# Performance work log

Measured on AMD Instinct MI355X. Metric: run time of the kernel, lower is better.

Reference implementation:

```python
import jax, jax.numpy as jnp
import numpy as np

N_NODES = 100000
N_EDGES = 3200000
F_IN, F_HID, F_OUT = 1433, 8, 7
K = 2  # kernel_size, dim=1, degree-1 B-spline -> basis (1-u, u)
LEAKY_SLOPE = 0.2


def att_spline_conv(x, edge_index, pseudo, w, root, att, bias, n_nodes):
    """Attention SplineConv layer (dim=1, kernel_size=2, linear B-spline).

    w:    [K, in, out] spline kernel weights
    root: [in, out]    root/self weight
    att:  [2*out]      attention vector (src-message part || dst part)
    """
    src, dst = edge_index[0], edge_index[1]
    u = pseudo[:, 0]                                   # [E], in [0,1]
    basis = jnp.stack([1.0 - u, u], axis=1)            # [E, K]
    # transform at node level first (cheap), then gather per edge
    xw = jnp.einsum('ni,kio->nko', x, w)               # [N, K, out]
    m = jnp.einsum('ek,eko->eo', basis, xw[src])       # [E, out] spline message
    h = x @ root                                       # [N, out] root transform
    out_dim = w.shape[-1]
    # GAT-style attention: leaky_relu(a_src . m_e + a_dst . h_dst)
    score = m @ att[:out_dim] + (h @ att[out_dim:])[dst]   # [E]
    score = jax.nn.leaky_relu(score, LEAKY_SLOPE)
    smax = jax.ops.segment_max(score, dst, num_segments=n_nodes)
    e = jnp.exp(score - smax[dst])
    denom = jax.ops.segment_sum(e, dst, num_segments=n_nodes)
    alpha = e / (denom[dst] + 1e-16)                   # segment softmax over dst
    agg = jax.ops.segment_sum(alpha[:, None] * m, dst, num_segments=n_nodes)
    return agg + h + bias


def setup_inputs() -> dict:
    key = jax.random.key(0)
    ks = jax.random.split(key, 12)
    x = jax.random.normal(ks[0], (N_NODES, F_IN), dtype=jnp.float32)
    edge_index = jax.random.randint(ks[1], (2, N_EDGES), 0, N_NODES, dtype=jnp.int64)
    pseudo = jax.random.uniform(ks[2], (N_EDGES, 1), dtype=jnp.float32)
    s1 = 1.0 / np.sqrt(F_IN)
    s2 = 1.0 / np.sqrt(F_HID)
    return {
        'x': x,
        'edge_index': edge_index,
        'pseudo': pseudo,
        'w1': jax.random.normal(ks[3], (K, F_IN, F_HID), dtype=jnp.float32) * s1,
        'root1': jax.random.normal(ks[4], (F_IN, F_HID), dtype=jnp.float32) * s1,
        'att1': jax.random.normal(ks[5], (2 * F_HID,), dtype=jnp.float32) * s2,
        'bias1': jnp.zeros((F_HID,), dtype=jnp.float32),
        'w2': jax.random.normal(ks[6], (K, F_HID, F_OUT), dtype=jnp.float32) * s2,
        'root2': jax.random.normal(ks[7], (F_HID, F_OUT), dtype=jnp.float32) * s2,
        'att2': jax.random.normal(ks[8], (2 * F_OUT,), dtype=jnp.float32) * s2,
        'bias2': jnp.zeros((F_OUT,), dtype=jnp.float32),
    }


def reference(x, edge_index, pseudo, w1, root1, att1, bias1, w2, root2, att2, bias2):
    # eval mode: F.dropout with training=False is identity
    n = x.shape[0]
    h = jax.nn.elu(att_spline_conv(x, edge_index, pseudo, w1, root1, att1, bias1, n))
    h = att_spline_conv(h, edge_index, pseudo, w2, root2, att2, bias2, n)
    return jax.nn.log_softmax(h, axis=1)
```

## Files before the change

kernel.cpp:

```cpp
#include <hip/hip_runtime.h>
#include <math.h>

#define TPB 256
#define F_IN 1433
#define KT 32
#define NKT 45
#define ROWS 128
#define XSTR 40
#define WSTR 40

typedef __attribute__((ext_vector_type(8))) short bf16x8;
typedef __attribute__((ext_vector_type(4))) float f32x4;

static __device__ __forceinline__ short f2bf(float f) {
    unsigned u = __float_as_uint(f);
    unsigned r = (u + 0x7FFFu + ((u >> 16) & 1u)) >> 16;
    return (short)r;
}

__global__ __launch_bounds__(256) void node1_hist_kernel(
    const float* __restrict__ x,
    const float* __restrict__ w1,
    const float* __restrict__ root1,
    const float* __restrict__ att1,
    float* __restrict__ XW1,
    float* __restrict__ H1,
    float2* __restrict__ SC1,
    float* __restrict__ HA1,
    const int* __restrict__ ei,
    int* __restrict__ cnt,
    int N, int E, int NB1)
{
    __shared__ short xbuf[2][ROWS][XSTR];
    __shared__ short wbuf[2][32][WSTR];

    const int tid = threadIdx.x;
    const int bid = blockIdx.x;

    if (bid >= NB1) {
        int e = (bid - NB1) * TPB + tid;
        if (e < E) atomicAdd(&cnt[ei[(size_t)E + e]], 1);
        return;
    }

    const int rowbase = bid * ROWS;
    const int wv   = tid >> 6;
    const int lane = tid & 63;

    for (int i = tid; i < 2 * 8 * WSTR; i += TPB) {
        int b = i / (8 * WSTR), r = i % (8 * WSTR);
        wbuf[b][24 + r / WSTR][r % WSTR] = 0;
    }

    auto stage = [&](int b, int c) {
        const int kb = c * KT;
        {
            int row = tid >> 1;
            int g = rowbase + row; if (g >= N) g = N - 1;
            int k0 = kb + (tid & 1) * 16;
            const float* src = x + (size_t)g * F_IN + k0;
            float v[16];
            if (k0 + 16 <= F_IN) {
#pragma unroll
                for (int q = 0; q < 4; ++q) {
                    float4 f = *reinterpret_cast<const float4*>(src + q * 4);
                    v[q * 4 + 0] = f.x; v[q * 4 + 1] = f.y;
                    v[q * 4 + 2] = f.z; v[q * 4 + 3] = f.w;
                }
            } else {
#pragma unroll
                for (int q = 0; q < 16; ++q) v[q] = (k0 + q < F_IN) ? src[q] : 0.f;
            }
            short* dst = &xbuf[b][row][(tid & 1) * 16];
#pragma unroll
            for (int h = 0; h < 2; ++h) {
                bf16x8 pk;
#pragma unroll
                for (int q = 0; q < 8; ++q) pk[q] = f2bf(v[h * 8 + q]);
                *reinterpret_cast<bf16x8*>(dst + h * 8) = pk;
            }
        }
#pragma unroll
        for (int i = 0; i < 3; ++i) {
            int e2 = tid + i * 256;
            int kl = e2 & 31, col = e2 >> 5;
            int k = kb + kl;
            float v = 0.f;
            if (k < F_IN) {
                if (col < 8)       v = w1[(size_t)k * 8 + col];
                else if (col < 16) v = w1[(size_t)(F_IN + k) * 8 + (col - 8)];
                else               v = root1[(size_t)k * 8 + (col - 16)];
            }
            wbuf[b][col][kl] = f2bf(v);
        }
    };

    f32x4 acc[2][2];
#pragma unroll
    for (int i = 0; i < 2; ++i)
#pragma unroll
        for (int j = 0; j < 2; ++j)
#pragma unroll
            for (int r = 0; r < 4; ++r) acc[i][j][r] = 0.f;

    stage(0, 0);
    __syncthreads();

    for (int c = 0; c < NKT; ++c) {
        int b = c & 1;
        if (c + 1 < NKT) stage(b ^ 1, c + 1);
        const int koff = (lane >> 4) * 8;
        bf16x8 a0 = *reinterpret_cast<const bf16x8*>(&xbuf[b][wv * 32 + (lane & 15)][koff]);
        bf16x8 a1 = *reinterpret_cast<const bf16x8*>(&xbuf[b][wv * 32 + 16 + (lane & 15)][koff]);
        bf16x8 b0 = *reinterpret_cast<const bf16x8*>(&wbuf[b][lane & 15][koff]);
        bf16x8 b1 = *reinterpret_cast<const bf16x8*>(&wbuf[b][16 + (lane & 15)][koff]);
        acc[0][0] = __builtin_amdgcn_mfma_f32_16x16x32_bf16(a0, b0, acc[0][0], 0, 0, 0);
        acc[0][1] = __builtin_amdgcn_mfma_f32_16x16x32_bf16(a0, b1, acc[0][1], 0, 0, 0);
        acc[1][0] = __builtin_amdgcn_mfma_f32_16x16x32_bf16(a1, b0, acc[1][0], 0, 0, 0);
        acc[1][1] = __builtin_amdgcn_mfma_f32_16x16x32_bf16(a1, b1, acc[1][1], 0, 0, 0);
        __syncthreads();
    }

    float* dump = reinterpret_cast<float*>(xbuf);
#pragma unroll
    for (int rt = 0; rt < 2; ++rt)
#pragma unroll
        for (int ot = 0; ot < 2; ++ot) {
            int col = ot * 16 + (lane & 15);
            if (col < 24) {
#pragma unroll
                for (int r = 0; r < 4; ++r) {
                    int row = wv * 32 + rt * 16 + (lane >> 4) * 4 + r;
                    dump[row * 25 + col] = acc[rt][ot][r];
                }
            }
        }
    __syncthreads();

    if (tid < ROWS) {
        int n = rowbase + tid;
        if (n < N) {
            float sum[24];
#pragma unroll
            for (int j = 0; j < 24; ++j) sum[j] = dump[tid * 25 + j];
            float s0 = 0.f, s1 = 0.f, ha = 0.f;
#pragma unroll
            for (int j = 0; j < 8; ++j) {
                s0 += sum[j] * att1[j];
                s1 += sum[8 + j] * att1[j];
                ha += sum[16 + j] * att1[8 + j];
            }
            float4* xwout = reinterpret_cast<float4*>(XW1 + (size_t)n * 16);
            xwout[0] = make_float4(sum[0], sum[1], sum[2], sum[3]);
            xwout[1] = make_float4(sum[4], sum[5], sum[6], sum[7]);
            xwout[2] = make_float4(sum[8], sum[9], sum[10], sum[11]);
            xwout[3] = make_float4(sum[12], sum[13], sum[14], sum[15]);
            float4* hout = reinterpret_cast<float4*>(H1 + (size_t)n * 8);
            hout[0] = make_float4(sum[16], sum[17], sum[18], sum[19]);
            hout[1] = make_float4(sum[20], sum[21], sum[22], sum[23]);
            SC1[n] = make_float2(s0, s1);
            HA1[n] = ha;
        }
    }
}

__global__ __launch_bounds__(256) void scanA_kernel(
    const int* __restrict__ cnt, int* __restrict__ rowptr, int* __restrict__ bsums, int N)
{
    __shared__ int lds[256];
    int t = threadIdx.x;
    int base = blockIdx.x * 1024 + t * 4;
    int c[4];
#pragma unroll
    for (int j = 0; j < 4; ++j) c[j] = (base + j < N) ? cnt[base + j] : 0;
    int tsum = c[0] + c[1] + c[2] + c[3];
    lds[t] = tsum;
    __syncthreads();
    for (int off = 1; off < 256; off <<= 1) {
        int v = (t >= off) ? lds[t - off] : 0;
        __syncthreads();
        lds[t] += v;
        __syncthreads();
    }
    int run = lds[t] - tsum;
#pragma unroll
    for (int j = 0; j < 4; ++j) {
        if (base + j < N) rowptr[base + j] = run;
        run += c[j];
    }
    if (t == 255) bsums[blockIdx.x] = lds[255];
}

__global__ __launch_bounds__(128) void scanB_kernel(int* __restrict__ bsums, int nb)
{
    __shared__ int lds[128];
    int t = threadIdx.x;
    int v = (t < nb) ? bsums[t] : 0;
    lds[t] = v;
    __syncthreads();
    for (int off = 1; off < 128; off <<= 1) {
        int w = (t >= off) ? lds[t - off] : 0;
        __syncthreads();
        lds[t] += w;
        __syncthreads();
    }
    if (t < nb) bsums[t] = lds[t] - v;
}

__global__ __launch_bounds__(256) void scanC_kernel(
    int* __restrict__ rowptr, int* __restrict__ cnt, const int* __restrict__ bsums, int N, int E)
{
    int i = blockIdx.x * TPB + threadIdx.x;
    if (i < N) {
        int v = rowptr[i] + bsums[i >> 10];
        rowptr[i] = v;
        cnt[i] = v;
    }
    if (i == 0) rowptr[N] = E;
}

__global__ __launch_bounds__(256) void scatter_kernel(
    const int* __restrict__ ei, const float* __restrict__ pseudo,
    int* __restrict__ cursor, int2* __restrict__ recs, int E)
{
    int e = blockIdx.x * TPB + threadIdx.x;
    if (e >= E) return;
    int s = ei[e];
    int d = ei[(size_t)E + e];
    float u = pseudo[e];
    int pos = atomicAdd(&cursor[d], 1);
    recs[pos] = make_int2(s, __float_as_int(u));
}

__global__ __launch_bounds__(256) void gather1_kernel(
    const int* __restrict__ rowptr, const int2* __restrict__ recs,
    const float4* __restrict__ XW1v,
    const float2* __restrict__ SC1, const float* __restrict__ HA1,
    const float* __restrict__ H1, const float* __restrict__ bias1,
    const float* __restrict__ w2, const float* __restrict__ root2, const float* __restrict__ att2,
    float* __restrict__ XW2, float* __restrict__ H2, float2* __restrict__ SC2, float* __restrict__ HA2,
    int N)
{
    int tid = blockIdx.x * TPB + threadIdx.x;
    int n = tid >> 4;
    int lane = tid & 15;
    if (n >= N) return;
    int start = rowptr[n], end = rowptr[n + 1];
    float ha = HA1[n];
    float den = 0.f;
    float num[8];
#pragma unroll
    for (int j = 0; j < 8; ++j) num[j] = 0.f;

    for (int i = start + lane; i < end; i += 16) {
        int2 r = recs[i];
        int s = r.x;
        float u = __int_as_float(r.y);
        float um = 1.f - u;
        float2 sc = SC1[s];
        float raw = um * sc.x + u * sc.y + ha;
        float score = (raw > 0.f) ? raw : 0.2f * raw;
        float w = expf(score);
        const float4* xw = XW1v + (size_t)s * 4;
        float4 p0 = xw[0], p1 = xw[1], q0 = xw[2], q1 = xw[3];
        num[0] = fmaf(w, um * p0.x + u * q0.x, num[0]);
        num[1] = fmaf(w, um * p0.y + u * q0.y, num[1]);
        num[2] = fmaf(w, um * p0.z + u * q0.z, num[2]);
        num[3] = fmaf(w, um * p0.w + u * q0.w, num[3]);
        num[4] = fmaf(w, um * p1.x + u * q1.x, num[4]);
        num[5] = fmaf(w, um * p1.y + u * q1.y, num[5]);
        num[6] = fmaf(w, um * p1.z + u * q1.z, num[6]);
        num[7] = fmaf(w, um * p1.w + u * q1.w, num[7]);
        den += w;
    }
#pragma unroll
    for (int off = 1; off < 16; off <<= 1) {
#pragma unroll
        for (int j = 0; j < 8; ++j) num[j] += __shfl_xor(num[j], off);
        den += __shfl_xor(den, off);
    }
    if (lane != 0) return;

    float inv = 1.f / (den + 1e-16f);
    float hp[8];
#pragma unroll
    for (int j = 0; j < 8; ++j) {
        float o = num[j] * inv + H1[(size_t)n * 8 + j] + bias1[j];
        hp[j] = (o > 0.f) ? o : expm1f(o);
    }
    float a[7], b[7], h[7];
#pragma unroll
    for (int j2 = 0; j2 < 7; ++j2) { a[j2] = 0.f; b[j2] = 0.f; h[j2] = 0.f; }
#pragma unroll
    for (int j = 0; j < 8; ++j) {
#pragma unroll
        for (int j2 = 0; j2 < 7; ++j2) {
            a[j2] = fmaf(hp[j], w2[j * 7 + j2], a[j2]);
            b[j2] = fmaf(hp[j], w2[56 + j * 7 + j2], b[j2]);
            h[j2] = fmaf(hp[j], root2[j * 7 + j2], h[j2]);
        }
    }
    float s0 = 0.f, s1 = 0.f, hA = 0.f;
#pragma unroll
    for (int j2 = 0; j2 < 7; ++j2) {
        s0 += a[j2] * att2[j2];
        s1 += b[j2] * att2[j2];
        hA += h[j2] * att2[7 + j2];
    }
    float4* xwout = reinterpret_cast<float4*>(XW2 + (size_t)n * 16);
    xwout[0] = make_float4(a[0], a[1], a[2], a[3]);
    xwout[1] = make_float4(a[4], a[5], a[6], 0.f);
    xwout[2] = make_float4(b[0], b[1], b[2], b[3]);
    xwout[3] = make_float4(b[4], b[5], b[6], 0.f);
    float4* hout = reinterpret_cast<float4*>(H2 + (size_t)n * 8);
    hout[0] = make_float4(h[0], h[1], h[2], h[3]);
    hout[1] = make_float4(h[4], h[5], h[6], 0.f);
    SC2[n] = make_float2(s0, s1);
    HA2[n] = hA;
}

__global__ __launch_bounds__(256) void gather2_kernel(
    const int* __restrict__ rowptr, const int2* __restrict__ recs,
    const float4* __restrict__ XW2v,
    const float2* __restrict__ SC2, const float* __restrict__ HA2,
    const float* __restrict__ H2, const float* __restrict__ bias2,
    float* __restrict__ out, int N)
{
    int tid = blockIdx.x * TPB + threadIdx.x;
    int n = tid >> 4;
    int lane = tid & 15;
    if (n >= N) return;
    int start = rowptr[n], end = rowptr[n + 1];
    float ha = HA2[n];
    float den = 0.f;
    float num[7];
#pragma unroll
    for (int j = 0; j < 7; ++j) num[j] = 0.f;

    for (int i = start + lane; i < end; i += 16) {
        int2 r = recs[i];
        int s = r.x;
        float u = __int_as_float(r.y);
        float um = 1.f - u;
        float2 sc = SC2[s];
        float raw = um * sc.x + u * sc.y + ha;
        float score = (raw > 0.f) ? raw : 0.2f * raw;
        float w = expf(score);
        const float4* xw = XW2v + (size_t)s * 4;
        float4 p0 = xw[0], p1 = xw[1], q0 = xw[2], q1 = xw[3];
        num[0] = fmaf(w, um * p0.x + u * q0.x, num[0]);
        num[1] = fmaf(w, um * p0.y + u * q0.y, num[1]);
        num[2] = fmaf(w, um * p0.z + u * q0.z, num[2]);
        num[3] = fmaf(w, um * p0.w + u * q0.w, num[3]);
        num[4] = fmaf(w, um * p1.x + u * q1.x, num[4]);
        num[5] = fmaf(w, um * p1.y + u * q1.y, num[5]);
        num[6] = fmaf(w, um * p1.z + u * q1.z, num[6]);
        den += w;
    }
#pragma unroll
    for (int off = 1; off < 16; off <<= 1) {
#pragma unroll
        for (int j = 0; j < 7; ++j) num[j] += __shfl_xor(num[j], off);
        den += __shfl_xor(den, off);
    }
    if (lane != 0) return;

    float inv = 1.f / (den + 1e-16f);
    float o[7];
    float mx = -1e30f;
#pragma unroll
    for (int j = 0; j < 7; ++j) {
        o[j] = fmaf(num[j], inv, H2[(size_t)n * 8 + j] + bias2[j]);
        mx = fmaxf(mx, o[j]);
    }
    float sum = 0.f;
#pragma unroll
    for (int j = 0; j < 7; ++j) sum += expf(o[j] - mx);
    float lse = mx + logf(sum);
#pragma unroll
    for (int j = 0; j < 7; ++j) out[(size_t)n * 7 + j] = o[j] - lse;
}

extern "C" void kernel_launch(void* const* d_in, const int* in_sizes, int n_in,
                              void* d_out, int out_size, void* d_ws, size_t ws_size,
                              hipStream_t stream) {
    const float* x      = (const float*)d_in[0];
    const int*   ei     = (const int*)d_in[1];
    const float* pseudo = (const float*)d_in[2];
    const float* w1     = (const float*)d_in[3];
    const float* root1  = (const float*)d_in[4];
    const float* att1   = (const float*)d_in[5];
    const float* bias1  = (const float*)d_in[6];
    const float* w2     = (const float*)d_in[7];
    const float* root2  = (const float*)d_in[8];
    const float* att2   = (const float*)d_in[9];
    const float* bias2  = (const float*)d_in[10];

    const int N = in_sizes[0] / F_IN;
    const int E = in_sizes[2];
    const size_t Ns = (size_t)N;

    float* ws   = (float*)d_ws;
    float* XW1  = ws;
    float* H1   = XW1 + 16 * Ns;
    float2* SC1 = (float2*)(H1 + 8 * Ns);
    float* HA1  = (float*)SC1 + 2 * Ns;
    float* XW2  = HA1 + Ns;
    float* H2   = XW2 + 16 * Ns;
    float2* SC2 = (float2*)(H2 + 8 * Ns);
    float* HA2  = (float*)SC2 + 2 * Ns;
    int*   cnt    = (int*)(HA2 + Ns);
    int*   rowptr = cnt + Ns;
    int*   bsums  = rowptr + Ns + 1;
    size_t off = (size_t)(bsums + 128) - (size_t)d_ws;
    off = (off + 7) & ~(size_t)7;
    int2*  recs = (int2*)((char*)d_ws + off);

    int nblk  = (N + TPB - 1) / TPB;
    int eblk  = (E + TPB - 1) / TPB;
    int sblkA = (N + 1023) / 1024;
    int nb1   = (N + ROWS - 1) / ROWS;
    int gblk  = ((N * 16) + TPB - 1) / TPB;

    hipMemsetAsync(cnt, 0, Ns * sizeof(int), stream);

    node1_hist_kernel<<<nb1 + eblk, TPB, 0, stream>>>(
        x, w1, root1, att1, XW1, H1, SC1, HA1, ei, cnt, N, E, nb1);
    scanA_kernel<<<sblkA, TPB, 0, stream>>>(cnt, rowptr, bsums, N);
    scanB_kernel<<<1, 128, 0, stream>>>(bsums, sblkA);
    scanC_kernel<<<nblk, TPB, 0, stream>>>(rowptr, cnt, bsums, N, E);
    scatter_kernel<<<eblk, TPB, 0, stream>>>(ei, pseudo, cnt, recs, E);
    gather1_kernel<<<gblk, TPB, 0, stream>>>(rowptr, recs, (const float4*)XW1, SC1, HA1,
                                             H1, bias1, w2, root2, att2,
                                             XW2, H2, SC2, HA2, N);
    gather2_kernel<<<gblk, TPB, 0, stream>>>(rowptr, recs, (const float4*)XW2, SC2, HA2,
                                             H2, bias2, (float*)d_out, N);
}
```

Baseline: 726.3 us.

## Load GEMM operands directly to registers and pre-transpose weights to bf16

The node-level x·[w1|root1] GEMM no longer stages x and weight tiles through double-buffered LDS with a __syncthreads per k-step. Each lane now loads its MFMA fragments straight from global memory into registers, with two-stage register prefetching. A new prep kernel packs the weights once per call into a transposed, padded bf16 layout so B fragments become single 16-byte loads. The aim is to remove LDS traffic and barriers from a memory-bound GEMM. The cost is uncoalesced-ish per-lane row reads of x (32-byte chunks per row), one extra kernel launch, and higher register pressure.

```diff
diff --git a/kernel.cpp b/kernel.cpp
--- a/kernel.cpp
+++ b/kernel.cpp
@@ -3,11 +3,9 @@
 
 #define TPB 256
 #define F_IN 1433
-#define KT 32
+#define KPAD 1440
 #define NKT 45
 #define ROWS 128
-#define XSTR 40
-#define WSTR 40
 
 typedef __attribute__((ext_vector_type(8))) short bf16x8;
 typedef __attribute__((ext_vector_type(4))) float f32x4;
@@ -18,10 +16,24 @@
     return (short)r;
 }
 
+__global__ __launch_bounds__(256) void prep_wt_kernel(
+    const float* __restrict__ w1, const float* __restrict__ root1, short* __restrict__ WT)
+{
+    int i = blockIdx.x * 256 + threadIdx.x;
+    if (i >= 32 * KPAD) return;
+    int col = i / KPAD, k = i - col * KPAD;
+    float v = 0.f;
+    if (k < F_IN) {
+        if (col < 8)       v = w1[(size_t)k * 8 + col];
+        else if (col < 16) v = w1[(size_t)(F_IN + k) * 8 + (col - 8)];
+        else if (col < 24) v = root1[(size_t)k * 8 + (col - 16)];
+    }
+    WT[i] = f2bf(v);
+}
+
 __global__ __launch_bounds__(256) void node1_hist_kernel(
     const float* __restrict__ x,
-    const float* __restrict__ w1,
-    const float* __restrict__ root1,
+    const short* __restrict__ WT,
     const float* __restrict__ att1,
     float* __restrict__ XW1,
     float* __restrict__ H1,
@@ -31,8 +43,7 @@
     int* __restrict__ cnt,
     int N, int E, int NB1)
 {
-    __shared__ short xbuf[2][ROWS][XSTR];
-    __shared__ short wbuf[2][32][WSTR];
+    __shared__ float dump[ROWS * 25];
 
     const int tid = threadIdx.x;
     const int bid = blockIdx.x;
@@ -43,85 +54,81 @@
         return;
     }
 
-    const int rowbase = bid * ROWS;
     const int wv   = tid >> 6;
     const int lane = tid & 63;
-
-    for (int i = tid; i < 2 * 8 * WSTR; i += TPB) {
-        int b = i / (8 * WSTR), r = i % (8 * WSTR);
-        wbuf[b][24 + r / WSTR][r % WSTR] = 0;
-    }
-
-    auto stage = [&](int b, int c) {
-        const int kb = c * KT;
-        {
-            int row = tid >> 1;
-            int g = rowbase + row; if (g >= N) g = N - 1;
-            int k0 = kb + (tid & 1) * 16;
-            const float* src = x + (size_t)g * F_IN + k0;
-            float v[16];
-            if (k0 + 16 <= F_IN) {
-#pragma unroll
-                for (int q = 0; q < 4; ++q) {
-                    float4 f = *reinterpret_cast<const float4*>(src + q * 4);
-                    v[q * 4 + 0] = f.x; v[q * 4 + 1] = f.y;
-                    v[q * 4 + 2] = f.z; v[q * 4 + 3] = f.w;
-                }
-            } else {
-#pragma unroll
-                for (int q = 0; q < 16; ++q) v[q] = (k0 + q < F_IN) ? src[q] : 0.f;
-            }
-            short* dst = &xbuf[b][row][(tid & 1) * 16];
-#pragma unroll
-            for (int h = 0; h < 2; ++h) {
-                bf16x8 pk;
-#pragma unroll
-                for (int q = 0; q < 8; ++q) pk[q] = f2bf(v[h * 8 + q]);
-                *reinterpret_cast<bf16x8*>(dst + h * 8) = pk;
-            }
+    const int rowbase = bid * ROWS;
+
+    int r0 = rowbase + wv * 32 + (lane & 15);
+    int r1 = r0 + 16;
+    if (r0 >= N) r0 = N - 1;
+    if (r1 >= N) r1 = N - 1;
+    const float* xr0 = x + (size_t)r0 * F_IN;
+    const float* xr1 = x + (size_t)r1 * F_IN;
+    const int klane = (lane >> 4) << 3;
+    const short* wt0 = WT + (size_t)(lane & 15) * KPAD;
+    const short* wt1 = wt0 + 16 * KPAD;
+
+    f32x4 acc[2][2];
+#pragma unroll
+    for (int i = 0; i < 2; ++i)
+#pragma unroll
+        for (int j = 0; j < 2; ++j)
+#pragma unroll
+            for (int r = 0; r < 4; ++r) acc[i][j][r] = 0.f;
+
+#define LOADA(c, A0, A1) do {                                                  \
+        int kf = (c) * 32 + klane;                                             \
+        if (kf + 8 <= F_IN) {                                                  \
+            float4 u0 = *reinterpret_cast<const float4*>(xr0 + kf);            \
+            float4 u1 = *reinterpret_cast<const float4*>(xr0 + kf + 4);        \
+            float4 v0 = *reinterpret_cast<const float4*>(xr1 + kf);            \
+            float4 v1 = *reinterpret_cast<const float4*>(xr1 + kf + 4);        \
+            A0[0] = u0.x; A0[1] = u0.y; A0[2] = u0.z; A0[3] = u0.w;            \
+            A0[4] = u1.x; A0[5] = u1.y; A0[6] = u1.z; A0[7] = u1.w;            \
+            A1[0] = v0.x; A1[1] = v0.y; A1[2] = v0.z; A1[3] = v0.w;            \
+            A1[4] = v1.x; A1[5] = v1.y; A1[6] = v1.z; A1[7] = v1.w;            \
+        } else {                                                               \
+            _Pragma("unroll")                                                  \
+            for (int q = 0; q < 8; ++q) {                                      \
+                A0[q] = (kf + q < F_IN) ? xr0[kf + q] : 0.f;                   \
+                A1[q] = (kf + q < F_IN) ? xr1[kf + q] : 0.f;                   \
+            }                                                                  \
+        }                                                                      \
+    } while (0)
+
+#define LOADB(c, B0, B1) do {                                                  \
+        int kf = (c) * 32 + klane;                                             \
+        B0 = *reinterpret_cast<const bf16x8*>(wt0 + kf);                       \
+        B1 = *reinterpret_cast<const bf16x8*>(wt1 + kf);                       \
+    } while (0)
+
+#define COMPUTE(A0, A1, B0, B1) do {                                           \
+        bf16x8 pa0, pa1;                                                       \
+        _Pragma("unroll")                                                      \
+        for (int q = 0; q < 8; ++q) { pa0[q] = f2bf(A0[q]); pa1[q] = f2bf(A1[q]); } \
+        acc[0][0] = __builtin_amdgcn_mfma_f32_16x16x32_bf16(pa0, B0, acc[0][0], 0, 0, 0); \
+        acc[0][1] = __builtin_amdgcn_mfma_f32_16x16x32_bf16(pa0, B1, acc[0][1], 0, 0, 0); \
+        acc[1][0] = __builtin_amdgcn_mfma_f32_16x16x32_bf16(pa1, B0, acc[1][0], 0, 0, 0); \
+        acc[1][1] = __builtin_amdgcn_mfma_f32_16x16x32_bf16(pa1, B1, acc[1][1], 0, 0, 0); \
+    } while (0)
+
+    float a0A[8], a1A[8], a0B[8], a1B[8];
+    bf16x8 b0A, b1A, b0B, b1B;
+
+    LOADA(0, a0A, a1A);
+    LOADB(0, b0A, b1A);
+    for (int c = 0; c < NKT; c += 2) {
+        if (c + 1 < NKT) { LOADA(c + 1, a0B, a1B); LOADB(c + 1, b0B, b1B); }
+        COMPUTE(a0A, a1A, b0A, b1A);
+        if (c + 1 < NKT) {
+            if (c + 2 < NKT) { LOADA(c + 2, a0A, a1A); LOADB(c + 2, b0A, b1A); }
+            COMPUTE(a0B, a1B, b0B, b1B);
         }
-#pragma unroll
-        for (int i = 0; i < 3; ++i) {
-            int e2 = tid + i * 256;
-            int kl = e2 & 31, col = e2 >> 5;
-            int k = kb + kl;
-            float v = 0.f;
-            if (k < F_IN) {
-                if (col < 8)       v = w1[(size_t)k * 8 + col];
-                else if (col < 16) v = w1[(size_t)(F_IN + k) * 8 + (col - 8)];
-                else               v = root1[(size_t)k * 8 + (col - 16)];
-            }
-            wbuf[b][col][kl] = f2bf(v);
-        }
-    };
-
-    f32x4 acc[2][2];
-#pragma unroll
-    for (int i = 0; i < 2; ++i)
-#pragma unroll
-        for (int j = 0; j < 2; ++j)
-#pragma unroll
-            for (int r = 0; r < 4; ++r) acc[i][j][r] = 0.f;
-
-    stage(0, 0);
-    __syncthreads();
-
-    for (int c = 0; c < NKT; ++c) {
-        int b = c & 1;
-        if (c + 1 < NKT) stage(b ^ 1, c + 1);
-        const int koff = (lane >> 4) * 8;
-        bf16x8 a0 = *reinterpret_cast<const bf16x8*>(&xbuf[b][wv * 32 + (lane & 15)][koff]);
-        bf16x8 a1 = *reinterpret_cast<const bf16x8*>(&xbuf[b][wv * 32 + 16 + (lane & 15)][koff]);
-        bf16x8 b0 = *reinterpret_cast<const bf16x8*>(&wbuf[b][lane & 15][koff]);
-        bf16x8 b1 = *reinterpret_cast<const bf16x8*>(&wbuf[b][16 + (lane & 15)][koff]);
-        acc[0][0] = __builtin_amdgcn_mfma_f32_16x16x32_bf16(a0, b0, acc[0][0], 0, 0, 0);
-        acc[0][1] = __builtin_amdgcn_mfma_f32_16x16x32_bf16(a0, b1, acc[0][1], 0, 0, 0);
-        acc[1][0] = __builtin_amdgcn_mfma_f32_16x16x32_bf16(a1, b0, acc[1][0], 0, 0, 0);
-        acc[1][1] = __builtin_amdgcn_mfma_f32_16x16x32_bf16(a1, b1, acc[1][1], 0, 0, 0);
-        __syncthreads();
-    }
-
-    float* dump = reinterpret_cast<float*>(xbuf);
+    }
+#undef LOADA
+#undef LOADB
+#undef COMPUTE
+
 #pragma unroll
     for (int rt = 0; rt < 2; ++rt)
 #pragma unroll
@@ -415,17 +422,22 @@
     size_t off = (size_t)(bsums + 128) - (size_t)d_ws;
     off = (off + 7) & ~(size_t)7;
     int2*  recs = (int2*)((char*)d_ws + off);
+    size_t woff = off + (size_t)E * sizeof(int2);
+    woff = (woff + 15) & ~(size_t)15;
+    short* WT = (short*)((char*)d_ws + woff);
 
     int nblk  = (N + TPB - 1) / TPB;
     int eblk  = (E + TPB - 1) / TPB;
     int sblkA = (N + 1023) / 1024;
     int nb1   = (N + ROWS - 1) / ROWS;
     int gblk  = ((N * 16) + TPB - 1) / TPB;
+    int wblk  = (32 * KPAD + TPB - 1) / TPB;
 
     hipMemsetAsync(cnt, 0, Ns * sizeof(int), stream);
 
+    prep_wt_kernel<<<wblk, TPB, 0, stream>>>(w1, root1, WT);
     node1_hist_kernel<<<nb1 + eblk, TPB, 0, stream>>>(
-        x, w1, root1, att1, XW1, H1, SC1, HA1, ei, cnt, N, E, nb1);
+        x, WT, att1, XW1, H1, SC1, HA1, ei, cnt, N, E, nb1);
     scanA_kernel<<<sblkA, TPB, 0, stream>>>(cnt, rowptr, bsums, N);
     scanB_kernel<<<1, 128, 0, stream>>>(bsums, sblkA);
     scanC_kernel<<<nblk, TPB, 0, stream>>>(rowptr, cnt, bsums, N, E);
```

New measurement: 644.8 us. 11.2% less time.

## Pre-convert spline weights to bf16 and use per-wave swizzled fp32 x staging

Applied to the files above, without the earlier changes.

A new prep kernel converts w1 and root1 once into a padded, transposed bf16 buffer and also zeroes the degree counters, which replaces the separate memset. The node GEMM now has each wave stage its own 32-row fp32 x tile in an XOR-swizzled shared-memory slice. It reads the weight fragments straight from global memory and converts x to bf16 at fragment-load time, so the block-wide barriers inside the K loop go away. The tail chunk is handled separately with bounds checks. The aim is to cut per-iteration weight reconversion and synchronisation so the x stream runs closer to memory bandwidth. The cost is an extra kernel launch and repeated per-wave weight loads from cache.

```diff
diff --git a/kernel.cpp b/kernel.cpp
--- a/kernel.cpp
+++ b/kernel.cpp
@@ -3,11 +3,10 @@
 
 #define TPB 256
 #define F_IN 1433
-#define KT 32
-#define NKT 45
+#define KPAD 1440
+#define NT 45
+#define NFULL 44
 #define ROWS 128
-#define XSTR 40
-#define WSTR 40
 
 typedef __attribute__((ext_vector_type(8))) short bf16x8;
 typedef __attribute__((ext_vector_type(4))) float f32x4;
@@ -18,10 +17,27 @@
     return (short)r;
 }
 
+__global__ __launch_bounds__(256) void prep_kernel(
+    const float* __restrict__ w1, const float* __restrict__ root1,
+    short* __restrict__ WT, int* __restrict__ cnt, int N)
+{
+    int i = blockIdx.x * 256 + threadIdx.x;
+    if (i < N) cnt[i] = 0;
+    if (i < 32 * KPAD) {
+        int col = i / KPAD, k = i - col * KPAD;
+        float v = 0.f;
+        if (k < F_IN) {
+            if (col < 8)       v = w1[(size_t)k * 8 + col];
+            else if (col < 16) v = w1[(size_t)(F_IN + k) * 8 + (col - 8)];
+            else if (col < 24) v = root1[(size_t)k * 8 + (col - 16)];
+        }
+        WT[i] = f2bf(v);
+    }
+}
+
 __global__ __launch_bounds__(256) void node1_hist_kernel(
     const float* __restrict__ x,
-    const float* __restrict__ w1,
-    const float* __restrict__ root1,
+    const short* __restrict__ WT,
     const float* __restrict__ att1,
     float* __restrict__ XW1,
     float* __restrict__ H1,
@@ -31,8 +47,7 @@
     int* __restrict__ cnt,
     int N, int E, int NB1)
 {
-    __shared__ short xbuf[2][ROWS][XSTR];
-    __shared__ short wbuf[2][32][WSTR];
+    __shared__ float xb[4][32][32];
 
     const int tid = threadIdx.x;
     const int bid = blockIdx.x;
@@ -43,57 +58,28 @@
         return;
     }
 
-    const int rowbase = bid * ROWS;
     const int wv   = tid >> 6;
     const int lane = tid & 63;
-
-    for (int i = tid; i < 2 * 8 * WSTR; i += TPB) {
-        int b = i / (8 * WSTR), r = i % (8 * WSTR);
-        wbuf[b][24 + r / WSTR][r % WSTR] = 0;
-    }
-
-    auto stage = [&](int b, int c) {
-        const int kb = c * KT;
-        {
-            int row = tid >> 1;
-            int g = rowbase + row; if (g >= N) g = N - 1;
-            int k0 = kb + (tid & 1) * 16;
-            const float* src = x + (size_t)g * F_IN + k0;
-            float v[16];
-            if (k0 + 16 <= F_IN) {
-#pragma unroll
-                for (int q = 0; q < 4; ++q) {
-                    float4 f = *reinterpret_cast<const float4*>(src + q * 4);
-                    v[q * 4 + 0] = f.x; v[q * 4 + 1] = f.y;
-                    v[q * 4 + 2] = f.z; v[q * 4 + 3] = f.w;
-                }
-            } else {
-#pragma unroll
-                for (int q = 0; q < 16; ++q) v[q] = (k0 + q < F_IN) ? src[q] : 0.f;
-            }
-            short* dst = &xbuf[b][row][(tid & 1) * 16];
-#pragma unroll
-            for (int h = 0; h < 2; ++h) {
-                bf16x8 pk;
-#pragma unroll
-                for (int q = 0; q < 8; ++q) pk[q] = f2bf(v[h * 8 + q]);
-                *reinterpret_cast<bf16x8*>(dst + h * 8) = pk;
-            }
-        }
-#pragma unroll
-        for (int i = 0; i < 3; ++i) {
-            int e2 = tid + i * 256;
-            int kl = e2 & 31, col = e2 >> 5;
-            int k = kb + kl;
-            float v = 0.f;
-            if (k < F_IN) {
-                if (col < 8)       v = w1[(size_t)k * 8 + col];
-                else if (col < 16) v = w1[(size_t)(F_IN + k) * 8 + (col - 8)];
-                else               v = root1[(size_t)k * 8 + (col - 16)];
-            }
-            wbuf[b][col][kl] = f2bf(v);
-        }
-    };
+    const int rowbase = bid * ROWS;
+
+    const int srow   = lane & 7;
+    const int schunk = lane >> 3;
+    const int pchunk = schunk ^ srow;
+    const float* gsrc[4];
+#pragma unroll
+    for (int g = 0; g < 4; ++g) {
+        int r = rowbase + wv * 32 + g * 8 + srow;
+        if (r >= N) r = N - 1;
+        gsrc[g] = x + (size_t)r * F_IN + schunk * 4;
+    }
+
+    const int r0 = lane & 15, r1 = r0 + 16;
+    const int klane = (lane >> 4) * 8;
+    const int c0 = klane >> 2;
+    const int p0 = c0 ^ (r0 & 7);
+    const int p1 = (c0 + 1) ^ (r0 & 7);
+    const short* wt0 = WT + (size_t)(lane & 15) * KPAD + klane;
+    const short* wt1 = wt0 + 16 * KPAD;
 
     f32x4 acc[2][2];
 #pragma unroll
@@ -103,25 +89,70 @@
 #pragma unroll
             for (int r = 0; r < 4; ++r) acc[i][j][r] = 0.f;
 
-    stage(0, 0);
+    {
+        float4 V[4];
+#pragma unroll
+        for (int g = 0; g < 4; ++g) V[g] = *reinterpret_cast<const float4*>(gsrc[g]);
+#pragma unroll
+        for (int g = 0; g < 4; ++g)
+            *reinterpret_cast<float4*>(&xb[wv][g * 8 + srow][pchunk * 4]) = V[g];
+    }
+
+    for (int t = 0; t < NFULL; ++t) {
+        float4 Vn[4];
+        const bool more = (t + 1 < NFULL);
+        if (more) {
+#pragma unroll
+            for (int g = 0; g < 4; ++g)
+                Vn[g] = *reinterpret_cast<const float4*>(gsrc[g] + (t + 1) * 32);
+        }
+        bf16x8 b0 = *reinterpret_cast<const bf16x8*>(wt0 + t * 32);
+        bf16x8 b1 = *reinterpret_cast<const bf16x8*>(wt1 + t * 32);
+        float4 fa0 = *reinterpret_cast<const float4*>(&xb[wv][r0][p0 * 4]);
+        float4 fb0 = *reinterpret_cast<const float4*>(&xb[wv][r0][p1 * 4]);
+        float4 fa1 = *reinterpret_cast<const float4*>(&xb[wv][r1][p0 * 4]);
+        float4 fb1 = *reinterpret_cast<const float4*>(&xb[wv][r1][p1 * 4]);
+        bf16x8 pa0, pa1;
+        pa0[0] = f2bf(fa0.x); pa0[1] = f2bf(fa0.y); pa0[2] = f2bf(fa0.z); pa0[3] = f2bf(fa0.w);
+        pa0[4] = f2bf(fb0.x); pa0[5] = f2bf(fb0.y); pa0[6] = f2bf(fb0.z); pa0[7] = f2bf(fb0.w);
+        pa1[0] = f2bf(fa1.x); pa1[1] = f2bf(fa1.y); pa1[2] = f2bf(fa1.z); pa1[3] = f2bf(fa1.w);
+        pa1[4] = f2bf(fb1.x); pa1[5] = f2bf(fb1.y); pa1[6] = f2bf(fb1.z); pa1[7] = f2bf(fb1.w);
+        acc[0][0] = __builtin_amdgcn_mfma_f32_16x16x32_bf16(pa0, b0, acc[0][0], 0, 0, 0);
+        acc[0][1] = __builtin_amdgcn_mfma_f32_16x16x32_bf16(pa0, b1, acc[0][1], 0, 0, 0);
+        acc[1][0] = __builtin_amdgcn_mfma_f32_16x16x32_bf16(pa1, b0, acc[1][0], 0, 0, 0);
+        acc[1][1] = __builtin_amdgcn_mfma_f32_16x16x32_bf16(pa1, b1, acc[1][1], 0, 0, 0);
+        if (more) {
+#pragma unroll
+            for (int g = 0; g < 4; ++g)
+                *reinterpret_cast<float4*>(&xb[wv][g * 8 + srow][pchunk * 4]) = Vn[g];
+        }
+    }
+
+    {
+        int rr0 = rowbase + wv * 32 + r0; if (rr0 >= N) rr0 = N - 1;
+        int rr1 = rowbase + wv * 32 + r1; if (rr1 >= N) rr1 = N - 1;
+        const float* xr0 = x + (size_t)rr0 * F_IN;
+        const float* xr1 = x + (size_t)rr1 * F_IN;
+        const int kf = NFULL * 32 + klane;
+        bf16x8 pa0, pa1;
+#pragma unroll
+        for (int q = 0; q < 8; ++q) {
+            float v0 = (kf + q < F_IN) ? xr0[kf + q] : 0.f;
+            float v1 = (kf + q < F_IN) ? xr1[kf + q] : 0.f;
+            pa0[q] = f2bf(v0);
+            pa1[q] = f2bf(v1);
+        }
+        bf16x8 b0 = *reinterpret_cast<const bf16x8*>(wt0 + NFULL * 32);
+        bf16x8 b1 = *reinterpret_cast<const bf16x8*>(wt1 + NFULL * 32);
+        acc[0][0] = __builtin_amdgcn_mfma_f32_16x16x32_bf16(pa0, b0, acc[0][0], 0, 0, 0);
+        acc[0][1] = __builtin_amdgcn_mfma_f32_16x16x32_bf16(pa0, b1, acc[0][1], 0, 0, 0);
+        acc[1][0] = __builtin_amdgcn_mfma_f32_16x16x32_bf16(pa1, b0, acc[1][0], 0, 0, 0);
+        acc[1][1] = __builtin_amdgcn_mfma_f32_16x16x32_bf16(pa1, b1, acc[1][1], 0, 0, 0);
+    }
+
     __syncthreads();
 
-    for (int c = 0; c < NKT; ++c) {
-        int b = c & 1;
-        if (c + 1 < NKT) stage(b ^ 1, c + 1);
-        const int koff = (lane >> 4) * 8;
-        bf16x8 a0 = *reinterpret_cast<const bf16x8*>(&xbuf[b][wv * 32 + (lane & 15)][koff]);
-        bf16x8 a1 = *reinterpret_cast<const bf16x8*>(&xbuf[b][wv * 32 + 16 + (lane & 15)][koff]);
-        bf16x8 b0 = *reinterpret_cast<const bf16x8*>(&wbuf[b][lane & 15][koff]);
-        bf16x8 b1 = *reinterpret_cast<const bf16x8*>(&wbuf[b][16 + (lane & 15)][koff]);
-        acc[0][0] = __builtin_amdgcn_mfma_f32_16x16x32_bf16(a0, b0, acc[0][0], 0, 0, 0);
-        acc[0][1] = __builtin_amdgcn_mfma_f32_16x16x32_bf16(a0, b1, acc[0][1], 0, 0, 0);
-        acc[1][0] = __builtin_amdgcn_mfma_f32_16x16x32_bf16(a1, b0, acc[1][0], 0, 0, 0);
-        acc[1][1] = __builtin_amdgcn_mfma_f32_16x16x32_bf16(a1, b1, acc[1][1], 0, 0, 0);
-        __syncthreads();
-    }
-
-    float* dump = reinterpret_cast<float*>(xbuf);
+    float* dump = reinterpret_cast<float*>(xb);
 #pragma unroll
     for (int rt = 0; rt < 2; ++rt)
 #pragma unroll
@@ -415,17 +446,21 @@
     size_t off = (size_t)(bsums + 128) - (size_t)d_ws;
     off = (off + 7) & ~(size_t)7;
     int2*  recs = (int2*)((char*)d_ws + off);
+    size_t woff = off + (size_t)E * sizeof(int2);
+    woff = (woff + 15) & ~(size_t)15;
+    short* WT = (short*)((char*)d_ws + woff);
 
     int nblk  = (N + TPB - 1) / TPB;
     int eblk  = (E + TPB - 1) / TPB;
     int sblkA = (N + 1023) / 1024;
     int nb1   = (N + ROWS - 1) / ROWS;
     int gblk  = ((N * 16) + TPB - 1) / TPB;
-
-    hipMemsetAsync(cnt, 0, Ns * sizeof(int), stream);
-
+    int prepn = (32 * KPAD > N) ? 32 * KPAD : N;
+    int pblk  = (prepn + TPB - 1) / TPB;
+
+    prep_kernel<<<pblk, TPB, 0, stream>>>(w1, root1, WT, cnt, N);
     node1_hist_kernel<<<nb1 + eblk, TPB, 0, stream>>>(
-        x, w1, root1, att1, XW1, H1, SC1, HA1, ei, cnt, N, E, nb1);
+        x, WT, att1, XW1, H1, SC1, HA1, ei, cnt, N, E, nb1);
     scanA_kernel<<<sblkA, TPB, 0, stream>>>(cnt, rowptr, bsums, N);
     scanB_kernel<<<1, 128, 0, stream>>>(bsums, sblkA);
     scanC_kernel<<<nblk, TPB, 0, stream>>>(rowptr, cnt, bsums, N, E);
```

Result: faster. 611.1 us (-15.9%).
